# Optimization experiments

Hardware: AMD Instinct MI355X
Metric: run time of the kernel (lower is better)

The kernel has to match this reference:

```python
import jax, jax.numpy as jnp
import numpy as np

N, K, D, V = 20000, 16, 256, 64  # nodes, neighbors, embed_dim, edge vocab


def setup_inputs() -> dict:
    key = jax.random.key(0)
    ks = jax.random.split(key, 16)
    s = 1.0 / np.sqrt(2 * D)  # Linear(512 -> 256) init scale
    return {
        "node_reps": jax.random.normal(ks[0], (1, N, D), jnp.float32),
        "in_indices": jax.random.randint(ks[1], (1, N, K), 0, N, jnp.int32),
        "in_edges": jax.random.randint(ks[2], (1, N, K), 0, V, jnp.int32),
        "in_mask": jax.random.uniform(ks[3], (1, N, K), jnp.float32),
        "out_indices": jax.random.randint(ks[4], (1, N, K), 0, N, jnp.int32),
        "out_edges": jax.random.randint(ks[5], (1, N, K), 0, V, jnp.int32),
        "out_mask": jax.random.uniform(ks[6], (1, N, K), jnp.float32),
        "edge_emb_1": jax.random.normal(ks[7], (V, D), jnp.float32),
        "W_1": jax.random.uniform(ks[8], (2 * D, D), jnp.float32, -s, s),
        "b_1": jnp.zeros((D,), jnp.float32),
        "edge_emb_2": jax.random.normal(ks[9], (V, D), jnp.float32),
        "W_2": jax.random.uniform(ks[10], (2 * D, D), jnp.float32, -s, s),
        "b_2": jnp.zeros((D,), jnp.float32),
        "edge_emb_3": jax.random.normal(ks[11], (V, D), jnp.float32),
        "W_3": jax.random.uniform(ks[12], (2 * D, D), jnp.float32, -s, s),
        "b_3": jnp.zeros((D,), jnp.float32),
    }


def gcn_layer(node_reps, in_idx, in_edg, in_msk, out_idx, out_edg, out_msk,
              edge_emb, W, b):
    # node_reps: [1, N, D]; dropout is identity in eval mode.
    nodes = node_reps[0]  # [N, D]; batch_size == 1 as in the original repo

    def agg(idx, edg, msk):
        nbr = nodes[idx]          # gather: [1, N, K, D]
        erep = edge_emb[edg]      # embedding lookup: [1, N, K, D]
        reps = jnp.concatenate([nbr, erep], axis=3) * msk[..., None]
        return reps.sum(axis=2)   # masked sum over neighbors: [1, N, 2D]

    in_reps = agg(in_idx, in_edg, in_msk)
    out_reps = agg(out_idx, out_edg, out_msk)
    in_nodes = in_reps[0] @ W + b    # [N, D]
    out_nodes = out_reps[0] @ W + b  # [N, D]
    return node_reps + out_nodes + in_nodes  # broadcast -> [1, N, D]


def reference(node_reps, in_indices, in_edges, in_mask,
              out_indices, out_edges, out_mask,
              edge_emb_1, W_1, b_1, edge_emb_2, W_2, b_2, edge_emb_3, W_3, b_3):
    nbrs = (in_indices, in_edges, in_mask, out_indices, out_edges, out_mask)
    hidden = gcn_layer(node_reps, *nbrs, edge_emb_1, W_1, b_1)  # gc1
    mu = gcn_layer(hidden, *nbrs, edge_emb_2, W_2, b_2)          # gc2
    logvar = gcn_layer(hidden, *nbrs, edge_emb_3, W_3, b_3)      # gc3

    mu_t = jnp.tanh(mu[0])        # [N, D]
    lv_t = jnp.tanh(logvar[0])    # [N, D]
    n_nodes = mu_t.shape[0]
    kld = (-0.5 / n_nodes) * jnp.mean(
        jnp.sum(1.0 + 2.0 * lv_t - mu_t ** 2 - jnp.exp(lv_t) ** 2, axis=1))
    return hidden, kld
```

## Files before the change

kernel.cpp:

```cpp
#include <hip/hip_runtime.h>
#include <math.h>

#define NN 20000
#define KK 16
#define DD 256
#define VV 64
#define NT1 16
#define SAS 336

typedef __attribute__((ext_vector_type(8))) __bf16 bf16x8;
typedef __attribute__((ext_vector_type(4))) float floatx4;
typedef __attribute__((ext_vector_type(2))) float floatx2;
typedef __attribute__((ext_vector_type(8))) unsigned short ushort8;
typedef __attribute__((ext_vector_type(4))) unsigned int uint4v;

__device__ __forceinline__ float4 ld4(const float* p) { return *reinterpret_cast<const float4*>(p); }

__device__ __forceinline__ unsigned short f2bf(float f) {
    union { float f; unsigned u; } v; v.f = f;
    unsigned r = v.u + 0x7FFFu + ((v.u >> 16) & 1u);
    return (unsigned short)(r >> 16);
}
__device__ __forceinline__ float bf2f(unsigned short u) {
    union { unsigned u; float f; } v; v.u = ((unsigned)u) << 16;
    return v.f;
}
__device__ __forceinline__ float bitf(unsigned u) {
    union { unsigned u; float f; } v; v.u = u;
    return v.f;
}
__device__ __forceinline__ unsigned char f2q(float f) {
    return (unsigned char)(__builtin_amdgcn_cvt_pk_fp8_f32(f, 0.f, 0u, false) & 0xFFu);
}
__device__ __forceinline__ float q2f(unsigned char q) {
    floatx2 r = __builtin_amdgcn_cvt_pk_f32_fp8((unsigned)q, false);
    return r.x;
}
__device__ __forceinline__ float ftanh(float v) {
    float e = __expf(2.f * v);
    return 1.f - 2.f * __builtin_amdgcn_rcpf(e + 1.f);
}

__global__ __launch_bounds__(256) void ewhist(
    const int* __restrict__ ie, const float* __restrict__ im,
    const int* __restrict__ oe, const float* __restrict__ om,
    const float* __restrict__ x,
    const float* __restrict__ e1, const float* __restrict__ W1,
    const float* __restrict__ e2, const float* __restrict__ W2,
    const float* __restrict__ e3, const float* __restrict__ W3,
    unsigned short* __restrict__ U1, unsigned short* __restrict__ U23,
    unsigned short* __restrict__ Hc, unsigned short* __restrict__ xh,
    float* __restrict__ kld) {
    int blk = blockIdx.x, tid = threadIdx.x;
    if (blk < 192) {
        int layer = blk >> 6, v = blk & 63, d = tid;
        const float* emb = layer == 0 ? e1 : (layer == 1 ? e2 : e3);
        const float* W   = layer == 0 ? W1 : (layer == 1 ? W2 : W3);
        float acc = 0.f;
        #pragma unroll 8
        for (int j = 0; j < 256; ++j)
            acc += emb[v * DD + j] * W[(size_t)(256 + j) * DD + d];
        unsigned short val = f2bf(acc);
        int j = v & 7, khi = (v >> 3) & 3, kt = 8 + (v >> 5);
        if (layer == 0) {
            int lane = khi * 16 + (d & 15), nt = d >> 4;
            U1[((size_t)(kt * 16 + nt) * 64 + lane) * 8 + j] = val;
        } else {
            int lane = khi * 16 + (d & 15);
            int nt = (layer == 1) ? (d >> 4) : 16 + (d >> 4);
            U23[((size_t)(kt * 32 + nt) * 64 + lane) * 8 + j] = val;
        }
    } else if (blk < 288) {
        int pblk = blk - 192;
        int u1path = pblk < 32;
        int g = (u1path ? pblk : pblk - 32) * 256 + tid;
        int lane = g & 63, ntk = g >> 6;
        int NT = u1path ? 16 : 32;
        int nt = ntk % NT, kt = ntk / NT;
        int n = nt * 16 + (lane & 15);
        int kbase = kt * 32 + (lane >> 4) * 8;
        const float* W = u1path ? W1 : (n < 256 ? W2 : W3);
        int nn = (n < 256) ? n : n - 256;
        unsigned short o8[8];
        #pragma unroll
        for (int j = 0; j < 8; ++j)
            o8[j] = f2bf(W[(size_t)(kbase + j) * DD + nn]);
        unsigned short* U = u1path ? U1 : U23;
        *reinterpret_cast<uint4v*>(&U[(size_t)g * 8]) = *reinterpret_cast<uint4v*>(o8);
    } else {
        int pb = blk - 288;
        int w = tid >> 6, lane = tid & 63;
        int n = pb * 4 + w;
        int e = 0; float m = 0.f;
        if (lane < 16)      { e = ie[n * KK + lane];      m = im[n * KK + lane]; }
        else if (lane < 32) { e = oe[n * KK + lane - 16]; m = om[n * KK + lane - 16]; }
        float h = 0.f;
        #pragma unroll
        for (int j = 0; j < 32; ++j) {
            int ev = __shfl(e, j);
            float mv = __shfl(m, j);
            if (ev == lane) h += mv;
        }
        Hc[(size_t)n * 64 + lane] = f2bf(h);
        size_t base = (size_t)pb * 1024 + tid * 4;
        float4 v = ld4(x + base);
        ushort4 o; o.x = f2bf(v.x); o.y = f2bf(v.y); o.z = f2bf(v.z); o.w = f2bf(v.w);
        *reinterpret_cast<ushort4*>(xh + base) = o;
        if (pb == 0 && tid == 0) *kld = 0.f;
    }
}

__global__ __launch_bounds__(256) void fmm1(const unsigned short* __restrict__ xh, const unsigned short* __restrict__ Hc,
                                            const int* __restrict__ ii, const float* __restrict__ im,
                                            const int* __restrict__ oi, const float* __restrict__ om,
                                            const unsigned short* __restrict__ U, const float* __restrict__ b,
                                            float* __restrict__ out, unsigned char* __restrict__ h8) {
    __shared__ unsigned short sA[16 * SAS];
    __shared__ int sidx[16][32];
    __shared__ float smsk[16][32];
    int n0 = blockIdx.x * 16;
    int tid = threadIdx.x;
    for (int q = tid; q < 512; q += 256) {
        int r = q >> 5, j = q & 31;
        int n = n0 + r;
        sidx[r][j] = (j < 16) ? ii[n * KK + j] : oi[n * KK + j - 16];
        smsk[r][j] = (j < 16) ? im[n * KK + j] : om[n * KK + j - 16];
    }
    if (tid < 128) {
        int r = tid >> 3, k8 = tid & 7;
        *reinterpret_cast<uint4v*>(&sA[r * SAS + 256 + k8 * 8]) =
            *reinterpret_cast<const uint4v*>(&Hc[(size_t)(n0 + r) * 64 + k8 * 8]);
    }
    __syncthreads();
    int lane = tid & 63, w = tid >> 6;
    int half = lane >> 5, c = (lane & 31) * 8;
    #pragma unroll
    for (int rr = 0; rr < 4; ++rr) {
        int row = w * 4 + rr;
        floatx2 zz = {0.f, 0.f};
        floatx2 acc2[4] = {zz, zz, zz, zz};
        #pragma unroll
        for (int j = 0; j < 16; ++j) {
            int j2 = j * 2 + half;
            int idx = sidx[row][j2];
            float m = smsk[row][j2];
            floatx2 m2 = {m, m};
            uint4v u = *reinterpret_cast<const uint4v*>(xh + (size_t)idx * DD + c);
            #pragma unroll
            for (int d = 0; d < 4; ++d) {
                unsigned uu = u[d];
                floatx2 p;
                p.x = bitf(uu << 16);
                p.y = bitf(uu & 0xFFFF0000u);
                acc2[d] += m2 * p;
            }
        }
        #pragma unroll
        for (int d = 0; d < 4; ++d) {
            acc2[d].x += __shfl_xor(acc2[d].x, 32);
            acc2[d].y += __shfl_xor(acc2[d].y, 32);
        }
        if (half == 0) {
            unsigned short o8[8];
            #pragma unroll
            for (int d = 0; d < 4; ++d) {
                o8[d * 2]     = f2bf(acc2[d].x);
                o8[d * 2 + 1] = f2bf(acc2[d].y);
            }
            *reinterpret_cast<uint4v*>(&sA[row * SAS + c]) = *reinterpret_cast<uint4v*>(o8);
        }
    }
    __syncthreads();
    int lr = lane & 15, quad = lane >> 4;
    float xp[4][4], bb[4];
    #pragma unroll
    for (int t = 0; t < 4; ++t) {
        int col = (w * 4 + t) * 16 + lr;
        bb[t] = 2.f * b[col];
        #pragma unroll
        for (int r = 0; r < 4; ++r)
            xp[t][r] = bf2f(xh[(size_t)(n0 + quad * 4 + r) * DD + col]);
    }
    floatx4 z = {0.f, 0.f, 0.f, 0.f};
    floatx4 acc[4] = {z, z, z, z};
    for (int kt = 0; kt < 10; ++kt) {
        bf16x8 a = *reinterpret_cast<const bf16x8*>(&sA[lr * SAS + kt * 32 + quad * 8]);
        #pragma unroll
        for (int t = 0; t < 4; ++t) {
            bf16x8 bf = *reinterpret_cast<const bf16x8*>(&U[(size_t)((kt * NT1 + w * 4 + t) * 64 + lane) * 8]);
            acc[t] = __builtin_amdgcn_mfma_f32_16x16x32_bf16(a, bf, acc[t], 0, 0, 0);
        }
    }
    #pragma unroll
    for (int t = 0; t < 4; ++t) {
        int col = (w * 4 + t) * 16 + lr;
        #pragma unroll
        for (int r = 0; r < 4; ++r) {
            size_t o = (size_t)(n0 + quad * 4 + r) * DD + col;
            float v = xp[t][r] + bb[t] + acc[t][r];
            out[o] = v;
            h8[o] = f2q(v);
        }
    }
}

__global__ __launch_bounds__(256) void fmm23(const unsigned char* __restrict__ h8, const unsigned short* __restrict__ Hc,
                                             const int* __restrict__ ii, const float* __restrict__ im,
                                             const int* __restrict__ oi, const float* __restrict__ om,
                                             const unsigned short* __restrict__ U, const float* __restrict__ b2,
                                             const float* __restrict__ b3, float* __restrict__ kld) {
    __shared__ unsigned short sA[16 * SAS];
    __shared__ int sidx[16][32];
    __shared__ float smsk[16][32];
    __shared__ float red[4];
    int n0 = blockIdx.x * 16;
    int tid = threadIdx.x;
    for (int q = tid; q < 512; q += 256) {
        int r = q >> 5, j = q & 31;
        int n = n0 + r;
        sidx[r][j] = (j < 16) ? ii[n * KK + j] : oi[n * KK + j - 16];
        smsk[r][j] = (j < 16) ? im[n * KK + j] : om[n * KK + j - 16];
    }
    if (tid < 128) {
        int r = tid >> 3, k8 = tid & 7;
        *reinterpret_cast<uint4v*>(&sA[r * SAS + 256 + k8 * 8]) =
            *reinterpret_cast<const uint4v*>(&Hc[(size_t)(n0 + r) * 64 + k8 * 8]);
    }
    __syncthreads();
    int lane = tid & 63, w = tid >> 6;
    int g = lane >> 4, cl = lane & 15;
    #pragma unroll
    for (int rr = 0; rr < 4; ++rr) {
        int row = w * 4 + rr;
        floatx2 zz = {0.f, 0.f};
        floatx2 acc2[8] = {zz, zz, zz, zz, zz, zz, zz, zz};
        #pragma unroll
        for (int j = 0; j < 8; ++j) {
            int r = g * 8 + j;
            int idx = sidx[row][r];
            float m = smsk[row][r];
            floatx2 m2 = {m, m};
            uint4v u = *reinterpret_cast<const uint4v*>(h8 + (size_t)idx * DD + cl * 16);
            #pragma unroll
            for (int d = 0; d < 4; ++d) {
                floatx2 f01 = __builtin_amdgcn_cvt_pk_f32_fp8(u[d], false);
                floatx2 f23 = __builtin_amdgcn_cvt_pk_f32_fp8(u[d], true);
                acc2[d * 2]     += m2 * f01;
                acc2[d * 2 + 1] += m2 * f23;
            }
        }
        #pragma unroll
        for (int z = 0; z < 8; ++z) {
            acc2[z].x += __shfl_xor(acc2[z].x, 16);
            acc2[z].y += __shfl_xor(acc2[z].y, 16);
            acc2[z].x += __shfl_xor(acc2[z].x, 32);
            acc2[z].y += __shfl_xor(acc2[z].y, 32);
        }
        if (g == 0) {
            unsigned short o16[16];
            #pragma unroll
            for (int d = 0; d < 4; ++d) {
                o16[d * 4 + 0] = f2bf(acc2[d * 2].x);
                o16[d * 4 + 1] = f2bf(acc2[d * 2].y);
                o16[d * 4 + 2] = f2bf(acc2[d * 2 + 1].x);
                o16[d * 4 + 3] = f2bf(acc2[d * 2 + 1].y);
            }
            uint4v* dst = reinterpret_cast<uint4v*>(&sA[row * SAS + cl * 16]);
            dst[0] = reinterpret_cast<uint4v*>(o16)[0];
            dst[1] = reinterpret_cast<uint4v*>(o16)[1];
        }
    }
    __syncthreads();
    int lr = lane & 15, quad = lane >> 4;
    float hp[4][4], bm[4], bl[4];
    #pragma unroll
    for (int t = 0; t < 4; ++t) {
        int col = (w * 4 + t) * 16 + lr;
        bm[t] = 2.f * b2[col];
        bl[t] = 2.f * b3[col];
        #pragma unroll
        for (int r = 0; r < 4; ++r)
            hp[t][r] = q2f(h8[(size_t)(n0 + quad * 4 + r) * DD + col]);
    }
    floatx4 z = {0.f, 0.f, 0.f, 0.f};
    floatx4 am[4] = {z, z, z, z};
    floatx4 al[4] = {z, z, z, z};
    for (int kt = 0; kt < 10; ++kt) {
        bf16x8 a = *reinterpret_cast<const bf16x8*>(&sA[lr * SAS + kt * 32 + quad * 8]);
        #pragma unroll
        for (int t = 0; t < 4; ++t) {
            int nt = w * 4 + t;
            bf16x8 bmu = *reinterpret_cast<const bf16x8*>(&U[(size_t)((kt * 32 + nt) * 64 + lane) * 8]);
            bf16x8 blv = *reinterpret_cast<const bf16x8*>(&U[(size_t)((kt * 32 + 16 + nt) * 64 + lane) * 8]);
            am[t] = __builtin_amdgcn_mfma_f32_16x16x32_bf16(a, bmu, am[t], 0, 0, 0);
            al[t] = __builtin_amdgcn_mfma_f32_16x16x32_bf16(a, blv, al[t], 0, 0, 0);
        }
    }
    float kacc = 0.f;
    #pragma unroll
    for (int t = 0; t < 4; ++t) {
        #pragma unroll
        for (int r = 0; r < 4; ++r) {
            float h = hp[t][r];
            float tm = ftanh(h + bm[t] + am[t][r]);
            float tl = ftanh(h + bl[t] + al[t][r]);
            kacc += (1.f - tm * tm) + (2.f * tl - __expf(2.f * tl));
        }
    }
    #pragma unroll
    for (int off = 32; off > 0; off >>= 1) kacc += __shfl_xor(kacc, off);
    if (lane == 0) red[w] = kacc;
    __syncthreads();
    if (tid == 0)
        atomicAdd(kld, (red[0] + red[1] + red[2] + red[3]) * (-0.5f / ((float)NN * (float)NN)));
}

extern "C" void kernel_launch(void* const* d_in, const int* in_sizes, int n_in,
                              void* d_out, int out_size, void* d_ws, size_t ws_size,
                              hipStream_t stream) {
    const float* x  = (const float*)d_in[0];
    const int*   ii = (const int*)d_in[1];
    const int*   ie = (const int*)d_in[2];
    const float* im = (const float*)d_in[3];
    const int*   oi = (const int*)d_in[4];
    const int*   oe = (const int*)d_in[5];
    const float* om = (const float*)d_in[6];
    const float* e1 = (const float*)d_in[7];
    const float* W1 = (const float*)d_in[8];
    const float* b1 = (const float*)d_in[9];
    const float* e2 = (const float*)d_in[10];
    const float* W2 = (const float*)d_in[11];
    const float* b2 = (const float*)d_in[12];
    const float* e3 = (const float*)d_in[13];
    const float* W3 = (const float*)d_in[14];
    const float* b3 = (const float*)d_in[15];
    float* out = (float*)d_out;
    float* kld = out + (size_t)NN * DD;

    char* ws = (char*)d_ws;
    unsigned short* U1  = (unsigned short*)(ws + 196608);
    unsigned short* U23 = (unsigned short*)(ws + 360448);
    unsigned short* Hc  = (unsigned short*)(ws + 688128);
    unsigned short* xh  = (unsigned short*)(ws + 3248128);
    unsigned char*  h8  = (unsigned char*)(ws + 13488128);

    ewhist<<<288 + NN / 4, 256, 0, stream>>>(ie, im, oe, om, x, e1, W1, e2, W2, e3, W3,
                                             U1, U23, Hc, xh, kld);
    fmm1  <<<NN / 16, 256, 0, stream>>>(xh, Hc, ii, im, oi, om, U1, b1, out, h8);
    fmm23 <<<NN / 16, 256, 0, stream>>>(h8, Hc, ii, im, oi, om, U23, b2, b3, kld);
}
```

Before: 190.3 us.

## Fuse three kernels into one persistent cooperative kernel with grid syncs

Merges the preprocessing, layer-1 and layer-2/3 kernels into a single persistent cooperative kernel. Blocks loop over virtual block and tile indices and are separated by grid-wide barriers. The aim is to remove the gaps between kernel launches. In exchange it adds grid-sync overhead, per-tile loop overhead, an occupancy query on every launch, and a grid capped at resident blocks, which can limit latency hiding in the gather phases.

```diff
diff --git a/kernel.cpp b/kernel.cpp
--- a/kernel.cpp
+++ b/kernel.cpp
@@ -1,4 +1,5 @@
 #include <hip/hip_runtime.h>
+#include <hip/hip_cooperative_groups.h>
 #include <math.h>
 
 #define NN 20000
@@ -7,6 +8,10 @@
 #define VV 64
 #define NT1 16
 #define SAS 336
+#define NTILE (NN / 16)
+#define NB_A (288 + NN / 4)
+
+namespace cg = cooperative_groups;
 
 typedef __attribute__((ext_vector_type(8))) __bf16 bf16x8;
 typedef __attribute__((ext_vector_type(4))) float floatx4;
@@ -41,278 +46,273 @@
     return 1.f - 2.f * __builtin_amdgcn_rcpf(e + 1.f);
 }
 
-__global__ __launch_bounds__(256) void ewhist(
-    const int* __restrict__ ie, const float* __restrict__ im,
-    const int* __restrict__ oe, const float* __restrict__ om,
+__global__ __launch_bounds__(256, 3) void vgae(
     const float* __restrict__ x,
-    const float* __restrict__ e1, const float* __restrict__ W1,
-    const float* __restrict__ e2, const float* __restrict__ W2,
-    const float* __restrict__ e3, const float* __restrict__ W3,
+    const int* __restrict__ ii, const int* __restrict__ ie, const float* __restrict__ im,
+    const int* __restrict__ oi, const int* __restrict__ oe, const float* __restrict__ om,
+    const float* __restrict__ e1, const float* __restrict__ W1, const float* __restrict__ b1,
+    const float* __restrict__ e2, const float* __restrict__ W2, const float* __restrict__ b2,
+    const float* __restrict__ e3, const float* __restrict__ W3, const float* __restrict__ b3,
     unsigned short* __restrict__ U1, unsigned short* __restrict__ U23,
     unsigned short* __restrict__ Hc, unsigned short* __restrict__ xh,
-    float* __restrict__ kld) {
-    int blk = blockIdx.x, tid = threadIdx.x;
-    if (blk < 192) {
-        int layer = blk >> 6, v = blk & 63, d = tid;
-        const float* emb = layer == 0 ? e1 : (layer == 1 ? e2 : e3);
-        const float* W   = layer == 0 ? W1 : (layer == 1 ? W2 : W3);
-        float acc = 0.f;
-        #pragma unroll 8
-        for (int j = 0; j < 256; ++j)
-            acc += emb[v * DD + j] * W[(size_t)(256 + j) * DD + d];
-        unsigned short val = f2bf(acc);
-        int j = v & 7, khi = (v >> 3) & 3, kt = 8 + (v >> 5);
-        if (layer == 0) {
-            int lane = khi * 16 + (d & 15), nt = d >> 4;
-            U1[((size_t)(kt * 16 + nt) * 64 + lane) * 8 + j] = val;
-        } else {
-            int lane = khi * 16 + (d & 15);
-            int nt = (layer == 1) ? (d >> 4) : 16 + (d >> 4);
-            U23[((size_t)(kt * 32 + nt) * 64 + lane) * 8 + j] = val;
-        }
-    } else if (blk < 288) {
-        int pblk = blk - 192;
-        int u1path = pblk < 32;
-        int g = (u1path ? pblk : pblk - 32) * 256 + tid;
-        int lane = g & 63, ntk = g >> 6;
-        int NT = u1path ? 16 : 32;
-        int nt = ntk % NT, kt = ntk / NT;
-        int n = nt * 16 + (lane & 15);
-        int kbase = kt * 32 + (lane >> 4) * 8;
-        const float* W = u1path ? W1 : (n < 256 ? W2 : W3);
-        int nn = (n < 256) ? n : n - 256;
-        unsigned short o8[8];
-        #pragma unroll
-        for (int j = 0; j < 8; ++j)
-            o8[j] = f2bf(W[(size_t)(kbase + j) * DD + nn]);
-        unsigned short* U = u1path ? U1 : U23;
-        *reinterpret_cast<uint4v*>(&U[(size_t)g * 8]) = *reinterpret_cast<uint4v*>(o8);
-    } else {
-        int pb = blk - 288;
-        int w = tid >> 6, lane = tid & 63;
-        int n = pb * 4 + w;
-        int e = 0; float m = 0.f;
-        if (lane < 16)      { e = ie[n * KK + lane];      m = im[n * KK + lane]; }
-        else if (lane < 32) { e = oe[n * KK + lane - 16]; m = om[n * KK + lane - 16]; }
-        float h = 0.f;
-        #pragma unroll
-        for (int j = 0; j < 32; ++j) {
-            int ev = __shfl(e, j);
-            float mv = __shfl(m, j);
-            if (ev == lane) h += mv;
-        }
-        Hc[(size_t)n * 64 + lane] = f2bf(h);
-        size_t base = (size_t)pb * 1024 + tid * 4;
-        float4 v = ld4(x + base);
-        ushort4 o; o.x = f2bf(v.x); o.y = f2bf(v.y); o.z = f2bf(v.z); o.w = f2bf(v.w);
-        *reinterpret_cast<ushort4*>(xh + base) = o;
-        if (pb == 0 && tid == 0) *kld = 0.f;
-    }
-}
-
-__global__ __launch_bounds__(256) void fmm1(const unsigned short* __restrict__ xh, const unsigned short* __restrict__ Hc,
-                                            const int* __restrict__ ii, const float* __restrict__ im,
-                                            const int* __restrict__ oi, const float* __restrict__ om,
-                                            const unsigned short* __restrict__ U, const float* __restrict__ b,
-                                            float* __restrict__ out, unsigned char* __restrict__ h8) {
-    __shared__ unsigned short sA[16 * SAS];
-    __shared__ int sidx[16][32];
-    __shared__ float smsk[16][32];
-    int n0 = blockIdx.x * 16;
-    int tid = threadIdx.x;
-    for (int q = tid; q < 512; q += 256) {
-        int r = q >> 5, j = q & 31;
-        int n = n0 + r;
-        sidx[r][j] = (j < 16) ? ii[n * KK + j] : oi[n * KK + j - 16];
-        smsk[r][j] = (j < 16) ? im[n * KK + j] : om[n * KK + j - 16];
-    }
-    if (tid < 128) {
-        int r = tid >> 3, k8 = tid & 7;
-        *reinterpret_cast<uint4v*>(&sA[r * SAS + 256 + k8 * 8]) =
-            *reinterpret_cast<const uint4v*>(&Hc[(size_t)(n0 + r) * 64 + k8 * 8]);
-    }
-    __syncthreads();
-    int lane = tid & 63, w = tid >> 6;
-    int half = lane >> 5, c = (lane & 31) * 8;
-    #pragma unroll
-    for (int rr = 0; rr < 4; ++rr) {
-        int row = w * 4 + rr;
-        floatx2 zz = {0.f, 0.f};
-        floatx2 acc2[4] = {zz, zz, zz, zz};
-        #pragma unroll
-        for (int j = 0; j < 16; ++j) {
-            int j2 = j * 2 + half;
-            int idx = sidx[row][j2];
-            float m = smsk[row][j2];
-            floatx2 m2 = {m, m};
-            uint4v u = *reinterpret_cast<const uint4v*>(xh + (size_t)idx * DD + c);
-            #pragma unroll
-            for (int d = 0; d < 4; ++d) {
-                unsigned uu = u[d];
-                floatx2 p;
-                p.x = bitf(uu << 16);
-                p.y = bitf(uu & 0xFFFF0000u);
-                acc2[d] += m2 * p;
-            }
-        }
-        #pragma unroll
-        for (int d = 0; d < 4; ++d) {
-            acc2[d].x += __shfl_xor(acc2[d].x, 32);
-            acc2[d].y += __shfl_xor(acc2[d].y, 32);
-        }
-        if (half == 0) {
-            unsigned short o8[8];
-            #pragma unroll
-            for (int d = 0; d < 4; ++d) {
-                o8[d * 2]     = f2bf(acc2[d].x);
-                o8[d * 2 + 1] = f2bf(acc2[d].y);
-            }
-            *reinterpret_cast<uint4v*>(&sA[row * SAS + c]) = *reinterpret_cast<uint4v*>(o8);
-        }
-    }
-    __syncthreads();
-    int lr = lane & 15, quad = lane >> 4;
-    float xp[4][4], bb[4];
-    #pragma unroll
-    for (int t = 0; t < 4; ++t) {
-        int col = (w * 4 + t) * 16 + lr;
-        bb[t] = 2.f * b[col];
-        #pragma unroll
-        for (int r = 0; r < 4; ++r)
-            xp[t][r] = bf2f(xh[(size_t)(n0 + quad * 4 + r) * DD + col]);
-    }
-    floatx4 z = {0.f, 0.f, 0.f, 0.f};
-    floatx4 acc[4] = {z, z, z, z};
-    for (int kt = 0; kt < 10; ++kt) {
-        bf16x8 a = *reinterpret_cast<const bf16x8*>(&sA[lr * SAS + kt * 32 + quad * 8]);
-        #pragma unroll
-        for (int t = 0; t < 4; ++t) {
-            bf16x8 bf = *reinterpret_cast<const bf16x8*>(&U[(size_t)((kt * NT1 + w * 4 + t) * 64 + lane) * 8]);
-            acc[t] = __builtin_amdgcn_mfma_f32_16x16x32_bf16(a, bf, acc[t], 0, 0, 0);
-        }
-    }
-    #pragma unroll
-    for (int t = 0; t < 4; ++t) {
-        int col = (w * 4 + t) * 16 + lr;
-        #pragma unroll
-        for (int r = 0; r < 4; ++r) {
-            size_t o = (size_t)(n0 + quad * 4 + r) * DD + col;
-            float v = xp[t][r] + bb[t] + acc[t][r];
-            out[o] = v;
-            h8[o] = f2q(v);
-        }
-    }
-}
-
-__global__ __launch_bounds__(256) void fmm23(const unsigned char* __restrict__ h8, const unsigned short* __restrict__ Hc,
-                                             const int* __restrict__ ii, const float* __restrict__ im,
-                                             const int* __restrict__ oi, const float* __restrict__ om,
-                                             const unsigned short* __restrict__ U, const float* __restrict__ b2,
-                                             const float* __restrict__ b3, float* __restrict__ kld) {
+    unsigned char* __restrict__ h8, float* __restrict__ out, float* __restrict__ kld) {
     __shared__ unsigned short sA[16 * SAS];
     __shared__ int sidx[16][32];
     __shared__ float smsk[16][32];
     __shared__ float red[4];
-    int n0 = blockIdx.x * 16;
-    int tid = threadIdx.x;
-    for (int q = tid; q < 512; q += 256) {
-        int r = q >> 5, j = q & 31;
-        int n = n0 + r;
-        sidx[r][j] = (j < 16) ? ii[n * KK + j] : oi[n * KK + j - 16];
-        smsk[r][j] = (j < 16) ? im[n * KK + j] : om[n * KK + j - 16];
+    const int tid = threadIdx.x;
+    const int gdim = gridDim.x;
+
+    for (int vb = blockIdx.x; vb < NB_A; vb += gdim) {
+        if (vb < 192) {
+            int layer = vb >> 6, v = vb & 63, d = tid;
+            const float* emb = layer == 0 ? e1 : (layer == 1 ? e2 : e3);
+            const float* W   = layer == 0 ? W1 : (layer == 1 ? W2 : W3);
+            float acc = 0.f;
+            #pragma unroll 8
+            for (int j = 0; j < 256; ++j)
+                acc += emb[v * DD + j] * W[(size_t)(256 + j) * DD + d];
+            unsigned short val = f2bf(acc);
+            int j = v & 7, khi = (v >> 3) & 3, kt = 8 + (v >> 5);
+            if (layer == 0) {
+                int lane = khi * 16 + (d & 15), nt = d >> 4;
+                U1[((size_t)(kt * 16 + nt) * 64 + lane) * 8 + j] = val;
+            } else {
+                int lane = khi * 16 + (d & 15);
+                int nt = (layer == 1) ? (d >> 4) : 16 + (d >> 4);
+                U23[((size_t)(kt * 32 + nt) * 64 + lane) * 8 + j] = val;
+            }
+        } else if (vb < 288) {
+            int pblk = vb - 192;
+            int u1path = pblk < 32;
+            int g = (u1path ? pblk : pblk - 32) * 256 + tid;
+            int lane = g & 63, ntk = g >> 6;
+            int NT = u1path ? 16 : 32;
+            int nt = ntk % NT, kt = ntk / NT;
+            int n = nt * 16 + (lane & 15);
+            int kbase = kt * 32 + (lane >> 4) * 8;
+            const float* W = u1path ? W1 : (n < 256 ? W2 : W3);
+            int nn = (n < 256) ? n : n - 256;
+            unsigned short o8[8];
+            #pragma unroll
+            for (int j = 0; j < 8; ++j)
+                o8[j] = f2bf(W[(size_t)(kbase + j) * DD + nn]);
+            unsigned short* U = u1path ? U1 : U23;
+            *reinterpret_cast<uint4v*>(&U[(size_t)g * 8]) = *reinterpret_cast<uint4v*>(o8);
+        } else {
+            int pb = vb - 288;
+            int w = tid >> 6, lane = tid & 63;
+            int n = pb * 4 + w;
+            int e = 0; float m = 0.f;
+            if (lane < 16)      { e = ie[n * KK + lane];      m = im[n * KK + lane]; }
+            else if (lane < 32) { e = oe[n * KK + lane - 16]; m = om[n * KK + lane - 16]; }
+            float h = 0.f;
+            #pragma unroll
+            for (int j = 0; j < 32; ++j) {
+                int ev = __shfl(e, j);
+                float mv = __shfl(m, j);
+                if (ev == lane) h += mv;
+            }
+            Hc[(size_t)n * 64 + lane] = f2bf(h);
+            size_t base = (size_t)pb * 1024 + tid * 4;
+            float4 v = ld4(x + base);
+            ushort4 o; o.x = f2bf(v.x); o.y = f2bf(v.y); o.z = f2bf(v.z); o.w = f2bf(v.w);
+            *reinterpret_cast<ushort4*>(xh + base) = o;
+            if (pb == 0 && tid == 0) *kld = 0.f;
+        }
     }
-    if (tid < 128) {
-        int r = tid >> 3, k8 = tid & 7;
-        *reinterpret_cast<uint4v*>(&sA[r * SAS + 256 + k8 * 8]) =
-            *reinterpret_cast<const uint4v*>(&Hc[(size_t)(n0 + r) * 64 + k8 * 8]);
+    cg::this_grid().sync();
+
+    for (int t = blockIdx.x; t < NTILE; t += gdim) {
+        int n0 = t * 16;
+        for (int q = tid; q < 512; q += 256) {
+            int r = q >> 5, j = q & 31;
+            int n = n0 + r;
+            sidx[r][j] = (j < 16) ? ii[n * KK + j] : oi[n * KK + j - 16];
+            smsk[r][j] = (j < 16) ? im[n * KK + j] : om[n * KK + j - 16];
+        }
+        if (tid < 128) {
+            int r = tid >> 3, k8 = tid & 7;
+            *reinterpret_cast<uint4v*>(&sA[r * SAS + 256 + k8 * 8]) =
+                *reinterpret_cast<const uint4v*>(&Hc[(size_t)(n0 + r) * 64 + k8 * 8]);
+        }
+        __syncthreads();
+        int lane = tid & 63, w = tid >> 6;
+        int half = lane >> 5, c = (lane & 31) * 8;
+        #pragma unroll
+        for (int rr = 0; rr < 4; ++rr) {
+            int row = w * 4 + rr;
+            floatx2 zz = {0.f, 0.f};
+            floatx2 acc2[4] = {zz, zz, zz, zz};
+            #pragma unroll
+            for (int j = 0; j < 16; ++j) {
+                int j2 = j * 2 + half;
+                int idx = sidx[row][j2];
+                float m = smsk[row][j2];
+                floatx2 m2 = {m, m};
+                uint4v u = *reinterpret_cast<const uint4v*>(xh + (size_t)idx * DD + c);
+                #pragma unroll
+                for (int d = 0; d < 4; ++d) {
+                    unsigned uu = u[d];
+                    floatx2 p;
+                    p.x = bitf(uu << 16);
+                    p.y = bitf(uu & 0xFFFF0000u);
+                    acc2[d] += m2 * p;
+                }
+            }
+            #pragma unroll
+            for (int d = 0; d < 4; ++d) {
+                acc2[d].x += __shfl_xor(acc2[d].x, 32);
+                acc2[d].y += __shfl_xor(acc2[d].y, 32);
+            }
+            if (half == 0) {
+                unsigned short o8[8];
+                #pragma unroll
+                for (int d = 0; d < 4; ++d) {
+                    o8[d * 2]     = f2bf(acc2[d].x);
+                    o8[d * 2 + 1] = f2bf(acc2[d].y);
+                }
+                *reinterpret_cast<uint4v*>(&sA[row * SAS + c]) = *reinterpret_cast<uint4v*>(o8);
+            }
+        }
+        __syncthreads();
+        int lr = lane & 15, quad = lane >> 4;
+        float xp[4][4], bb[4];
+        #pragma unroll
+        for (int t4 = 0; t4 < 4; ++t4) {
+            int col = (w * 4 + t4) * 16 + lr;
+            bb[t4] = 2.f * b1[col];
+            #pragma unroll
+            for (int r = 0; r < 4; ++r)
+                xp[t4][r] = bf2f(xh[(size_t)(n0 + quad * 4 + r) * DD + col]);
+        }
+        floatx4 z = {0.f, 0.f, 0.f, 0.f};
+        floatx4 acc[4] = {z, z, z, z};
+        for (int kt = 0; kt < 10; ++kt) {
+            bf16x8 a = *reinterpret_cast<const bf16x8*>(&sA[lr * SAS + kt * 32 + quad * 8]);
+            #pragma unroll
+            for (int t4 = 0; t4 < 4; ++t4) {
+                bf16x8 bf = *reinterpret_cast<const bf16x8*>(&U1[(size_t)((kt * NT1 + w * 4 + t4) * 64 + lane) * 8]);
+                acc[t4] = __builtin_amdgcn_mfma_f32_16x16x32_bf16(a, bf, acc[t4], 0, 0, 0);
+            }
+        }
+        #pragma unroll
+        for (int t4 = 0; t4 < 4; ++t4) {
+            int col = (w * 4 + t4) * 16 + lr;
+            #pragma unroll
+            for (int r = 0; r < 4; ++r) {
+                size_t o = (size_t)(n0 + quad * 4 + r) * DD + col;
+                float v = xp[t4][r] + bb[t4] + acc[t4][r];
+                out[o] = v;
+                h8[o] = f2q(v);
+            }
+        }
+        __syncthreads();
     }
-    __syncthreads();
-    int lane = tid & 63, w = tid >> 6;
-    int g = lane >> 4, cl = lane & 15;
-    #pragma unroll
-    for (int rr = 0; rr < 4; ++rr) {
-        int row = w * 4 + rr;
-        floatx2 zz = {0.f, 0.f};
-        floatx2 acc2[8] = {zz, zz, zz, zz, zz, zz, zz, zz};
-        #pragma unroll
-        for (int j = 0; j < 8; ++j) {
-            int r = g * 8 + j;
-            int idx = sidx[row][r];
-            float m = smsk[row][r];
-            floatx2 m2 = {m, m};
-            uint4v u = *reinterpret_cast<const uint4v*>(h8 + (size_t)idx * DD + cl * 16);
-            #pragma unroll
-            for (int d = 0; d < 4; ++d) {
-                floatx2 f01 = __builtin_amdgcn_cvt_pk_f32_fp8(u[d], false);
-                floatx2 f23 = __builtin_amdgcn_cvt_pk_f32_fp8(u[d], true);
-                acc2[d * 2]     += m2 * f01;
-                acc2[d * 2 + 1] += m2 * f23;
-            }
-        }
-        #pragma unroll
-        for (int z = 0; z < 8; ++z) {
-            acc2[z].x += __shfl_xor(acc2[z].x, 16);
-            acc2[z].y += __shfl_xor(acc2[z].y, 16);
-            acc2[z].x += __shfl_xor(acc2[z].x, 32);
-            acc2[z].y += __shfl_xor(acc2[z].y, 32);
-        }
-        if (g == 0) {
-            unsigned short o16[16];
-            #pragma unroll
-            for (int d = 0; d < 4; ++d) {
-                o16[d * 4 + 0] = f2bf(acc2[d * 2].x);
-                o16[d * 4 + 1] = f2bf(acc2[d * 2].y);
-                o16[d * 4 + 2] = f2bf(acc2[d * 2 + 1].x);
-                o16[d * 4 + 3] = f2bf(acc2[d * 2 + 1].y);
-            }
-            uint4v* dst = reinterpret_cast<uint4v*>(&sA[row * SAS + cl * 16]);
-            dst[0] = reinterpret_cast<uint4v*>(o16)[0];
-            dst[1] = reinterpret_cast<uint4v*>(o16)[1];
-        }
+    cg::this_grid().sync();
+
+    for (int t = blockIdx.x; t < NTILE; t += gdim) {
+        int n0 = t * 16;
+        for (int q = tid; q < 512; q += 256) {
+            int r = q >> 5, j = q & 31;
+            int n = n0 + r;
+            sidx[r][j] = (j < 16) ? ii[n * KK + j] : oi[n * KK + j - 16];
+            smsk[r][j] = (j < 16) ? im[n * KK + j] : om[n * KK + j - 16];
+        }
+        if (tid < 128) {
+            int r = tid >> 3, k8 = tid & 7;
+            *reinterpret_cast<uint4v*>(&sA[r * SAS + 256 + k8 * 8]) =
+                *reinterpret_cast<const uint4v*>(&Hc[(size_t)(n0 + r) * 64 + k8 * 8]);
+        }
+        __syncthreads();
+        int lane = tid & 63, w = tid >> 6;
+        int g = lane >> 4, cl = lane & 15;
+        #pragma unroll
+        for (int rr = 0; rr < 4; ++rr) {
+            int row = w * 4 + rr;
+            floatx2 zz = {0.f, 0.f};
+            floatx2 acc2[8] = {zz, zz, zz, zz, zz, zz, zz, zz};
+            #pragma unroll
+            for (int j = 0; j < 8; ++j) {
+                int r = g * 8 + j;
+                int idx = sidx[row][r];
+                float m = smsk[row][r];
+                floatx2 m2 = {m, m};
+                uint4v u = *reinterpret_cast<const uint4v*>(h8 + (size_t)idx * DD + cl * 16);
+                #pragma unroll
+                for (int d = 0; d < 4; ++d) {
+                    floatx2 f01 = __builtin_amdgcn_cvt_pk_f32_fp8(u[d], false);
+                    floatx2 f23 = __builtin_amdgcn_cvt_pk_f32_fp8(u[d], true);
+                    acc2[d * 2]     += m2 * f01;
+                    acc2[d * 2 + 1] += m2 * f23;
+                }
+            }
+            #pragma unroll
+            for (int zi = 0; zi < 8; ++zi) {
+                acc2[zi].x += __shfl_xor(acc2[zi].x, 16);
+                acc2[zi].y += __shfl_xor(acc2[zi].y, 16);
+                acc2[zi].x += __shfl_xor(acc2[zi].x, 32);
+                acc2[zi].y += __shfl_xor(acc2[zi].y, 32);
+            }
+            if (g == 0) {
+                unsigned short o16[16];
+                #pragma unroll
+                for (int d = 0; d < 4; ++d) {
+                    o16[d * 4 + 0] = f2bf(acc2[d * 2].x);
+                    o16[d * 4 + 1] = f2bf(acc2[d * 2].y);
+                    o16[d * 4 + 2] = f2bf(acc2[d * 2 + 1].x);
+                    o16[d * 4 + 3] = f2bf(acc2[d * 2 + 1].y);
+                }
+                uint4v* dst = reinterpret_cast<uint4v*>(&sA[row * SAS + cl * 16]);
+                dst[0] = reinterpret_cast<uint4v*>(o16)[0];
+                dst[1] = reinterpret_cast<uint4v*>(o16)[1];
+            }
+        }
+        __syncthreads();
+        int lr = lane & 15, quad = lane >> 4;
+        float hp[4][4], bm[4], bl[4];
+        #pragma unroll
+        for (int t4 = 0; t4 < 4; ++t4) {
+            int col = (w * 4 + t4) * 16 + lr;
+            bm[t4] = 2.f * b2[col];
+            bl[t4] = 2.f * b3[col];
+            #pragma unroll
+            for (int r = 0; r < 4; ++r)
+                hp[t4][r] = q2f(h8[(size_t)(n0 + quad * 4 + r) * DD + col]);
+        }
+        floatx4 z = {0.f, 0.f, 0.f, 0.f};
+        floatx4 am[4] = {z, z, z, z};
+        floatx4 al[4] = {z, z, z, z};
+        for (int kt = 0; kt < 10; ++kt) {
+            bf16x8 a = *reinterpret_cast<const bf16x8*>(&sA[lr * SAS + kt * 32 + quad * 8]);
+            #pragma unroll
+            for (int t4 = 0; t4 < 4; ++t4) {
+                int nt = w * 4 + t4;
+                bf16x8 bmu = *reinterpret_cast<const bf16x8*>(&U23[(size_t)((kt * 32 + nt) * 64 + lane) * 8]);
+                bf16x8 blv = *reinterpret_cast<const bf16x8*>(&U23[(size_t)((kt * 32 + 16 + nt) * 64 + lane) * 8]);
+                am[t4] = __builtin_amdgcn_mfma_f32_16x16x32_bf16(a, bmu, am[t4], 0, 0, 0);
+                al[t4] = __builtin_amdgcn_mfma_f32_16x16x32_bf16(a, blv, al[t4], 0, 0, 0);
+            }
+        }
+        float kacc = 0.f;
+        #pragma unroll
+        for (int t4 = 0; t4 < 4; ++t4) {
+            #pragma unroll
+            for (int r = 0; r < 4; ++r) {
+                float h = hp[t4][r];
+                float tm = ftanh(h + bm[t4] + am[t4][r]);
+                float tl = ftanh(h + bl[t4] + al[t4][r]);
+                kacc += (1.f - tm * tm) + (2.f * tl - __expf(2.f * tl));
+            }
+        }
+        #pragma unroll
+        for (int off = 32; off > 0; off >>= 1) kacc += __shfl_xor(kacc, off);
+        if (lane == 0) red[w] = kacc;
+        __syncthreads();
+        if (tid == 0)
+            atomicAdd(kld, (red[0] + red[1] + red[2] + red[3]) * (-0.5f / ((float)NN * (float)NN)));
+        __syncthreads();
     }
-    __syncthreads();
-    int lr = lane & 15, quad = lane >> 4;
-    float hp[4][4], bm[4], bl[4];
-    #pragma unroll
-    for (int t = 0; t < 4; ++t) {
-        int col = (w * 4 + t) * 16 + lr;
-        bm[t] = 2.f * b2[col];
-        bl[t] = 2.f * b3[col];
-        #pragma unroll
-        for (int r = 0; r < 4; ++r)
-            hp[t][r] = q2f(h8[(size_t)(n0 + quad * 4 + r) * DD + col]);
-    }
-    floatx4 z = {0.f, 0.f, 0.f, 0.f};
-    floatx4 am[4] = {z, z, z, z};
-    floatx4 al[4] = {z, z, z, z};
-    for (int kt = 0; kt < 10; ++kt) {
-        bf16x8 a = *reinterpret_cast<const bf16x8*>(&sA[lr * SAS + kt * 32 + quad * 8]);
-        #pragma unroll
-        for (int t = 0; t < 4; ++t) {
-            int nt = w * 4 + t;
-            bf16x8 bmu = *reinterpret_cast<const bf16x8*>(&U[(size_t)((kt * 32 + nt) * 64 + lane) * 8]);
-            bf16x8 blv = *reinterpret_cast<const bf16x8*>(&U[(size_t)((kt * 32 + 16 + nt) * 64 + lane) * 8]);
-            am[t] = __builtin_amdgcn_mfma_f32_16x16x32_bf16(a, bmu, am[t], 0, 0, 0);
-            al[t] = __builtin_amdgcn_mfma_f32_16x16x32_bf16(a, blv, al[t], 0, 0, 0);
-        }
-    }
-    float kacc = 0.f;
-    #pragma unroll
-    for (int t = 0; t < 4; ++t) {
-        #pragma unroll
-        for (int r = 0; r < 4; ++r) {
-            float h = hp[t][r];
-            float tm = ftanh(h + bm[t] + am[t][r]);
-            float tl = ftanh(h + bl[t] + al[t][r]);
-            kacc += (1.f - tm * tm) + (2.f * tl - __expf(2.f * tl));
-        }
-    }
-    #pragma unroll
-    for (int off = 32; off > 0; off >>= 1) kacc += __shfl_xor(kacc, off);
-    if (lane == 0) red[w] = kacc;
-    __syncthreads();
-    if (tid == 0)
-        atomicAdd(kld, (red[0] + red[1] + red[2] + red[3]) * (-0.5f / ((float)NN * (float)NN)));
 }
 
 extern "C" void kernel_launch(void* const* d_in, const int* in_sizes, int n_in,
@@ -344,8 +344,18 @@
     unsigned short* xh  = (unsigned short*)(ws + 3248128);
     unsigned char*  h8  = (unsigned char*)(ws + 13488128);
 
-    ewhist<<<288 + NN / 4, 256, 0, stream>>>(ie, im, oe, om, x, e1, W1, e2, W2, e3, W3,
-                                             U1, U23, Hc, xh, kld);
-    fmm1  <<<NN / 16, 256, 0, stream>>>(xh, Hc, ii, im, oi, om, U1, b1, out, h8);
-    fmm23 <<<NN / 16, 256, 0, stream>>>(h8, Hc, ii, im, oi, om, U23, b2, b3, kld);
-}
+    int maxb = 0;
+    hipOccupancyMaxActiveBlocksPerMultiprocessor(&maxb, (const void*)vgae, 256, 0);
+    if (maxb < 1) maxb = 1;
+    long long grid = (long long)maxb * 256;
+    if (grid > NTILE) grid = NTILE;
+
+    void* args[] = {
+        (void*)&x, (void*)&ii, (void*)&ie, (void*)&im, (void*)&oi, (void*)&oe, (void*)&om,
+        (void*)&e1, (void*)&W1, (void*)&b1, (void*)&e2, (void*)&W2, (void*)&b2,
+        (void*)&e3, (void*)&W3, (void*)&b3,
+        (void*)&U1, (void*)&U23, (void*)&Hc, (void*)&xh, (void*)&h8, (void*)&out, (void*)&kld
+    };
+    hipLaunchCooperativeKernel((const void*)vgae, dim3((unsigned)grid), dim3(256),
+                               args, 0, stream);
+}
```

New measurement: 568.4 us. 199% more time.

## Use 32-row tiles with 512 threads so each B fragment feeds two MFMAs

Applied to the files above, without the earlier changes.

Both fused gather+GEMM kernels now handle 32 nodes per block with 8 waves. Each wave computes two row tiles against two column tiles, so every weight fragment loaded from global memory is reused for two MFMAs, halving weight traffic per node. Residual and bias loads move after the MFMA loop to lower register pressure, and the fp32 output uses nontemporal stores. In exchange the kernels use more shared memory per block and have half as many blocks.

```diff
diff --git a/kernel.cpp b/kernel.cpp
--- a/kernel.cpp
+++ b/kernel.cpp
@@ -110,23 +110,23 @@
     }
 }
 
-__global__ __launch_bounds__(256) void fmm1(const unsigned short* __restrict__ xh, const unsigned short* __restrict__ Hc,
+__global__ __launch_bounds__(512) void fmm1(const unsigned short* __restrict__ xh, const unsigned short* __restrict__ Hc,
                                             const int* __restrict__ ii, const float* __restrict__ im,
                                             const int* __restrict__ oi, const float* __restrict__ om,
                                             const unsigned short* __restrict__ U, const float* __restrict__ b,
                                             float* __restrict__ out, unsigned char* __restrict__ h8) {
-    __shared__ unsigned short sA[16 * SAS];
-    __shared__ int sidx[16][32];
-    __shared__ float smsk[16][32];
-    int n0 = blockIdx.x * 16;
+    __shared__ unsigned short sA[32 * SAS];
+    __shared__ int sidx[32][32];
+    __shared__ float smsk[32][32];
+    int n0 = blockIdx.x * 32;
     int tid = threadIdx.x;
-    for (int q = tid; q < 512; q += 256) {
+    for (int q = tid; q < 1024; q += 512) {
         int r = q >> 5, j = q & 31;
         int n = n0 + r;
         sidx[r][j] = (j < 16) ? ii[n * KK + j] : oi[n * KK + j - 16];
         smsk[r][j] = (j < 16) ? im[n * KK + j] : om[n * KK + j - 16];
     }
-    if (tid < 128) {
+    if (tid < 256) {
         int r = tid >> 3, k8 = tid & 7;
         *reinterpret_cast<uint4v*>(&sA[r * SAS + 256 + k8 * 8]) =
             *reinterpret_cast<const uint4v*>(&Hc[(size_t)(n0 + r) * 64 + k8 * 8]);
@@ -172,56 +172,54 @@
     }
     __syncthreads();
     int lr = lane & 15, quad = lane >> 4;
-    float xp[4][4], bb[4];
-    #pragma unroll
-    for (int t = 0; t < 4; ++t) {
-        int col = (w * 4 + t) * 16 + lr;
-        bb[t] = 2.f * b[col];
-        #pragma unroll
-        for (int r = 0; r < 4; ++r)
-            xp[t][r] = bf2f(xh[(size_t)(n0 + quad * 4 + r) * DD + col]);
-    }
     floatx4 z = {0.f, 0.f, 0.f, 0.f};
-    floatx4 acc[4] = {z, z, z, z};
+    floatx4 acc[2][2] = {{z, z}, {z, z}};
     for (int kt = 0; kt < 10; ++kt) {
-        bf16x8 a = *reinterpret_cast<const bf16x8*>(&sA[lr * SAS + kt * 32 + quad * 8]);
-        #pragma unroll
-        for (int t = 0; t < 4; ++t) {
-            bf16x8 bf = *reinterpret_cast<const bf16x8*>(&U[(size_t)((kt * NT1 + w * 4 + t) * 64 + lane) * 8]);
-            acc[t] = __builtin_amdgcn_mfma_f32_16x16x32_bf16(a, bf, acc[t], 0, 0, 0);
-        }
-    }
-    #pragma unroll
-    for (int t = 0; t < 4; ++t) {
-        int col = (w * 4 + t) * 16 + lr;
-        #pragma unroll
-        for (int r = 0; r < 4; ++r) {
-            size_t o = (size_t)(n0 + quad * 4 + r) * DD + col;
-            float v = xp[t][r] + bb[t] + acc[t][r];
-            out[o] = v;
-            h8[o] = f2q(v);
-        }
-    }
-}
-
-__global__ __launch_bounds__(256) void fmm23(const unsigned char* __restrict__ h8, const unsigned short* __restrict__ Hc,
+        bf16x8 a0 = *reinterpret_cast<const bf16x8*>(&sA[lr * SAS + kt * 32 + quad * 8]);
+        bf16x8 a1 = *reinterpret_cast<const bf16x8*>(&sA[(16 + lr) * SAS + kt * 32 + quad * 8]);
+        #pragma unroll
+        for (int t = 0; t < 2; ++t) {
+            int nt = w * 2 + t;
+            bf16x8 bf = *reinterpret_cast<const bf16x8*>(&U[(size_t)((kt * NT1 + nt) * 64 + lane) * 8]);
+            acc[0][t] = __builtin_amdgcn_mfma_f32_16x16x32_bf16(a0, bf, acc[0][t], 0, 0, 0);
+            acc[1][t] = __builtin_amdgcn_mfma_f32_16x16x32_bf16(a1, bf, acc[1][t], 0, 0, 0);
+        }
+    }
+    #pragma unroll
+    for (int t = 0; t < 2; ++t) {
+        int col = (w * 2 + t) * 16 + lr;
+        float bb = 2.f * b[col];
+        #pragma unroll
+        for (int rt = 0; rt < 2; ++rt) {
+            #pragma unroll
+            for (int r = 0; r < 4; ++r) {
+                size_t o = (size_t)(n0 + rt * 16 + quad * 4 + r) * DD + col;
+                float v = bf2f(xh[o]) + bb + acc[rt][t][r];
+                __builtin_nontemporal_store(v, &out[o]);
+                h8[o] = f2q(v);
+            }
+        }
+    }
+}
+
+__global__ __launch_bounds__(512) void fmm23(const unsigned char* __restrict__ h8, const unsigned short* __restrict__ Hc,
                                              const int* __restrict__ ii, const float* __restrict__ im,
                                              const int* __restrict__ oi, const float* __restrict__ om,
                                              const unsigned short* __restrict__ U, const float* __restrict__ b2,
                                              const float* __restrict__ b3, float* __restrict__ kld) {
-    __shared__ unsigned short sA[16 * SAS];
-    __shared__ int sidx[16][32];
-    __shared__ float smsk[16][32];
-    __shared__ float red[4];
-    int n0 = blockIdx.x * 16;
+    __shared__ unsigned short sA[32 * SAS];
+    __shared__ int sidx[32][32];
+    __shared__ float smsk[32][32];
+    __shared__ float red[8];
+    int n0 = blockIdx.x * 32;
     int tid = threadIdx.x;
-    for (int q = tid; q < 512; q += 256) {
+    for (int q = tid; q < 1024; q += 512) {
         int r = q >> 5, j = q & 31;
         int n = n0 + r;
         sidx[r][j] = (j < 16) ? ii[n * KK + j] : oi[n * KK + j - 16];
         smsk[r][j] = (j < 16) ? im[n * KK + j] : om[n * KK + j - 16];
     }
-    if (tid < 128) {
+    if (tid < 256) {
         int r = tid >> 3, k8 = tid & 7;
         *reinterpret_cast<uint4v*>(&sA[r * SAS + 256 + k8 * 8]) =
             *reinterpret_cast<const uint4v*>(&Hc[(size_t)(n0 + r) * 64 + k8 * 8]);
@@ -272,47 +270,48 @@
     }
     __syncthreads();
     int lr = lane & 15, quad = lane >> 4;
-    float hp[4][4], bm[4], bl[4];
-    #pragma unroll
-    for (int t = 0; t < 4; ++t) {
-        int col = (w * 4 + t) * 16 + lr;
-        bm[t] = 2.f * b2[col];
-        bl[t] = 2.f * b3[col];
-        #pragma unroll
-        for (int r = 0; r < 4; ++r)
-            hp[t][r] = q2f(h8[(size_t)(n0 + quad * 4 + r) * DD + col]);
-    }
     floatx4 z = {0.f, 0.f, 0.f, 0.f};
-    floatx4 am[4] = {z, z, z, z};
-    floatx4 al[4] = {z, z, z, z};
+    floatx4 am[2][2] = {{z, z}, {z, z}};
+    floatx4 al[2][2] = {{z, z}, {z, z}};
     for (int kt = 0; kt < 10; ++kt) {
-        bf16x8 a = *reinterpret_cast<const bf16x8*>(&sA[lr * SAS + kt * 32 + quad * 8]);
-        #pragma unroll
-        for (int t = 0; t < 4; ++t) {
-            int nt = w * 4 + t;
+        bf16x8 a0 = *reinterpret_cast<const bf16x8*>(&sA[lr * SAS + kt * 32 + quad * 8]);
+        bf16x8 a1 = *reinterpret_cast<const bf16x8*>(&sA[(16 + lr) * SAS + kt * 32 + quad * 8]);
+        #pragma unroll
+        for (int t = 0; t < 2; ++t) {
+            int nt = w * 2 + t;
             bf16x8 bmu = *reinterpret_cast<const bf16x8*>(&U[(size_t)((kt * 32 + nt) * 64 + lane) * 8]);
             bf16x8 blv = *reinterpret_cast<const bf16x8*>(&U[(size_t)((kt * 32 + 16 + nt) * 64 + lane) * 8]);
-            am[t] = __builtin_amdgcn_mfma_f32_16x16x32_bf16(a, bmu, am[t], 0, 0, 0);
-            al[t] = __builtin_amdgcn_mfma_f32_16x16x32_bf16(a, blv, al[t], 0, 0, 0);
+            am[0][t] = __builtin_amdgcn_mfma_f32_16x16x32_bf16(a0, bmu, am[0][t], 0, 0, 0);
+            am[1][t] = __builtin_amdgcn_mfma_f32_16x16x32_bf16(a1, bmu, am[1][t], 0, 0, 0);
+            al[0][t] = __builtin_amdgcn_mfma_f32_16x16x32_bf16(a0, blv, al[0][t], 0, 0, 0);
+            al[1][t] = __builtin_amdgcn_mfma_f32_16x16x32_bf16(a1, blv, al[1][t], 0, 0, 0);
         }
     }
     float kacc = 0.f;
     #pragma unroll
-    for (int t = 0; t < 4; ++t) {
-        #pragma unroll
-        for (int r = 0; r < 4; ++r) {
-            float h = hp[t][r];
-            float tm = ftanh(h + bm[t] + am[t][r]);
-            float tl = ftanh(h + bl[t] + al[t][r]);
-            kacc += (1.f - tm * tm) + (2.f * tl - __expf(2.f * tl));
+    for (int t = 0; t < 2; ++t) {
+        int col = (w * 2 + t) * 16 + lr;
+        float bm = 2.f * b2[col];
+        float bl = 2.f * b3[col];
+        #pragma unroll
+        for (int rt = 0; rt < 2; ++rt) {
+            #pragma unroll
+            for (int r = 0; r < 4; ++r) {
+                float h = q2f(h8[(size_t)(n0 + rt * 16 + quad * 4 + r) * DD + col]);
+                float tm = ftanh(h + bm + am[rt][t][r]);
+                float tl = ftanh(h + bl + al[rt][t][r]);
+                kacc += (1.f - tm * tm) + (2.f * tl - __expf(2.f * tl));
+            }
         }
     }
     #pragma unroll
     for (int off = 32; off > 0; off >>= 1) kacc += __shfl_xor(kacc, off);
     if (lane == 0) red[w] = kacc;
     __syncthreads();
-    if (tid == 0)
-        atomicAdd(kld, (red[0] + red[1] + red[2] + red[3]) * (-0.5f / ((float)NN * (float)NN)));
+    if (tid == 0) {
+        float s = red[0] + red[1] + red[2] + red[3] + red[4] + red[5] + red[6] + red[7];
+        atomicAdd(kld, s * (-0.5f / ((float)NN * (float)NN)));
+    }
 }
 
 extern "C" void kernel_launch(void* const* d_in, const int* in_sizes, int n_in,
@@ -346,6 +345,6 @@
 
     ewhist<<<288 + NN / 4, 256, 0, stream>>>(ie, im, oe, om, x, e1, W1, e2, W2, e3, W3,
                                              U1, U23, Hc, xh, kld);
-    fmm1  <<<NN / 16, 256, 0, stream>>>(xh, Hc, ii, im, oi, om, U1, b1, out, h8);
-    fmm23 <<<NN / 16, 256, 0, stream>>>(h8, Hc, ii, im, oi, om, U23, b2, b3, kld);
-}
+    fmm1  <<<NN / 32, 512, 0, stream>>>(xh, Hc, ii, im, oi, om, U1, b1, out, h8);
+    fmm23 <<<NN / 32, 512, 0, stream>>>(h8, Hc, ii, im, oi, om, U23, b2, b3, kld);
+}
```

Result: no change. 189.3 us (-0.5%).
